# Kernel optimization log

Measured on AMD Instinct MI355X. Metric: run time of the kernel, lower is better.

## Reference

```python
import jax, jax.numpy as jnp
import numpy as np

N_HEADS = 16
EMBED_DIM = 2048
BATCH, SEQ = 2, 2048


def setup_inputs() -> dict:
    key = jax.random.key(0)
    k1, k2, k3, k4, k5 = jax.random.split(key, 5)
    s_in = 1.0 / np.sqrt(EMBED_DIM)
    return {
        "x": jax.random.normal(k1, (BATCH, SEQ, EMBED_DIM), dtype=jnp.float32),
        "w_in": jax.random.normal(k2, (3 * EMBED_DIM, EMBED_DIM), dtype=jnp.float32) * s_in,
        "b_in": jax.random.normal(k3, (3 * EMBED_DIM,), dtype=jnp.float32) * 0.02,
        "w_out": jax.random.normal(k4, (EMBED_DIM, EMBED_DIM), dtype=jnp.float32) * s_in,
        "b_out": jax.random.normal(k5, (EMBED_DIM,), dtype=jnp.float32) * 0.02,
        "causal_mask": 1,
    }


def reference(x, w_in, b_in, w_out, b_out, causal_mask):
    b, l, e = x.shape
    h, d = N_HEADS, e // N_HEADS
    qkv = x @ w_in.T + b_in                      # [b, l, 3e]
    q, k, v = jnp.split(qkv, 3, axis=-1)
    # b l (h d) -> b h l d
    q = q.reshape(b, l, h, d).transpose(0, 2, 1, 3)
    k = k.reshape(b, l, h, d).transpose(0, 2, 1, 3)
    v = v.reshape(b, l, h, d).transpose(0, 2, 1, 3)
    scores = jnp.einsum("bhqd,bhkd->bhqk", q, k) / jnp.sqrt(jnp.float32(d))
    if causal_mask:
        tri = jnp.triu(jnp.ones((l, l), dtype=bool), k=1)  # True above diagonal
        scores = jnp.where(tri, -jnp.inf, scores)
    attn = jax.nn.softmax(scores, axis=-1)
    out = jnp.einsum("bhqk,bhkd->bhqd", attn, v)  # [b, h, l, d]
    out = out.transpose(0, 2, 1, 3).reshape(b, l, e)
    return out @ w_out.T + b_out
```

## Files before the change

### kernel.cpp

```cpp
#include <hip/hip_runtime.h>
#include <hip/hip_bf16.h>
#include <math.h>

typedef __attribute__((ext_vector_type(4))) float floatx4;
typedef __attribute__((ext_vector_type(16))) float floatx16;
typedef __attribute__((ext_vector_type(8))) __bf16 bf16x8;

__device__ __forceinline__ unsigned short f2bf(float f) {
    union { float f; unsigned int u; } v; v.f = f;
    unsigned int u = v.u;
    u += 0x7FFFu + ((u >> 16) & 1u);
    return (unsigned short)(u >> 16);
}

__device__ __forceinline__ unsigned int pkbf(float a, float b) {
    return (unsigned int)f2bf(a) | ((unsigned int)f2bf(b) << 16);
}

__device__ __forceinline__ void gl_lds16(const void* g, void* l) {
    __builtin_amdgcn_global_load_lds(
        (const __attribute__((address_space(1))) void*)g,
        (__attribute__((address_space(3))) void*)l, 16, 0, 0);
}

__global__ void cast_f32_bf16(const float* __restrict__ in,
                              unsigned short* __restrict__ out, int n) {
    int i = (blockIdx.x * blockDim.x + threadIdx.x) * 4;
    if (i + 4 <= n) {
        float4 f = *(const float4*)(in + i);
        ushort4 o;
        o.x = f2bf(f.x); o.y = f2bf(f.y); o.z = f2bf(f.z); o.w = f2bf(f.w);
        *(ushort4*)(out + i) = o;
    }
}


#define VMCNT(n) asm volatile("s_waitcnt vmcnt(" #n ")" ::: "memory")
#define LGKM0()  asm volatile("s_waitcnt lgkmcnt(0)" ::: "memory")
#define BARF()   do { asm volatile("" ::: "memory"); __builtin_amdgcn_s_barrier(); \
                      asm volatile("" ::: "memory"); } while (0)

#define STAGE_A4(bsel, tt, h) do { \
    const unsigned short* _s = Ab + (size_t)((h) * 128 + rstage) * K + (tt) * 64 + scol; \
    char* _d = bufc + (bsel) * 49152 + (h) * 16384 + wid * 1024; \
    gl_lds16(_s, _d); \
    gl_lds16(_s + (size_t)64 * K, _d + 8192); \
} while (0)

#define STAGE_B4(bsel, tt, h) do { \
    const unsigned short* _s = Bb + (size_t)((h) * 64 + rstage) * K + (tt) * 64 + scol; \
    char* _d = bufc + (bsel) * 49152 + 32768 + (h) * 8192 + wid * 1024; \
    gl_lds16(_s, _d); \
} while (0)

#define STAGE_TILE(bsel, tt) do { \
    STAGE_A4(bsel, tt, 0); STAGE_A4(bsel, tt, 1); \
    STAGE_B4(bsel, tt, 0); STAGE_B4(bsel, tt, 1); \
} while (0)

#define RDA(base, ii, kse) (*(const bf16x8*)((base) + (ii) * 2048 + rdoffA + (kse)))
#define RDB(base, jj, kse) (*(const bf16x8*)((base) + (jj) * 2048 + rdoffB + (kse)))

#define MFMA_C(iofs) do { \
    __builtin_amdgcn_s_setprio(1); \
    _Pragma("unroll") \
    for (int ii = 0; ii < 4; ++ii) { \
        _Pragma("unroll") \
        for (int jj = 0; jj < 2; ++jj) { \
            acc[(iofs) + ii][jj] = __builtin_amdgcn_mfma_f32_16x16x32_bf16( \
                aF[((iofs) + ii) * 2 + 0], bL[jj * 2 + 0], acc[(iofs) + ii][jj], 0, 0, 0); \
            acc[(iofs) + ii][jj] = __builtin_amdgcn_mfma_f32_16x16x32_bf16( \
                aF[((iofs) + ii) * 2 + 1], bL[jj * 2 + 1], acc[(iofs) + ii][jj], 0, 0, 0); \
        } } \
    __builtin_amdgcn_s_setprio(0); \
} while (0)

template<int MODE>
__global__ __launch_bounds__(512, 2) void gemm4p(
    const unsigned short* __restrict__ A,
    const unsigned short* __restrict__ B,
    const float* __restrict__ bias,
    float* __restrict__ Cf,
    unsigned short* __restrict__ q_ws,
    unsigned short* __restrict__ k_ws,
    unsigned short* __restrict__ vT_ws,
    int M, int N, int K)
{
    extern __shared__ char ldsc[];
    char* const bufc = ldsc;

    const int nby = M >> 8;
    const int nwg = gridDim.x;
    const int qq = nwg >> 3;
    const int wg = (blockIdx.x & 7) * qq + (blockIdx.x >> 3);
    const int by = wg % nby, bx = wg / nby;
    const int m0 = by << 8, n0 = bx << 7;

    const int tid = threadIdx.x;
    const int lane = tid & 63, wid = tid >> 6;
    const int li = lane & 15, quad = lane >> 4;
    const int wr = wid >> 2, wc = wid & 3;

    const int rstage = tid >> 3;
    const int scol = (((tid & 7) ^ ((tid >> 3) & 7)) << 3);
    const unsigned short* Ab = A + (size_t)m0 * K;
    const unsigned short* Bb = B + (size_t)n0 * K;

    const int swz = (lane & 7) << 4;
    const int ks0 = ((quad << 4)     ) ^ swz;
    const int ks1 = ((quad << 4) + 64) ^ swz;
    const int rdoffA = li * 128;
    const int rdoffB = li * 128 + ((wc & 1) << 12);

    const char* rdA0 = bufc + wr * 16384;
    const char* rdB0 = bufc + 32768 + (wc >> 1) * 8192;
    const char* rdA1 = rdA0 + 49152;
    const char* rdB1 = rdB0 + 49152;

    floatx4 acc[8][2] = {};
    bf16x8 aF[16], bL[4];

    const int KTn = K >> 6;

    STAGE_TILE(0, 0);
    STAGE_TILE(1, 1);
    VMCNT(6);
    BARF();

    for (int t = 0; t < KTn; t += 2) {
        const bool pf = (t + 2 < KTn);

        #pragma unroll
        for (int ii = 0; ii < 8; ++ii) { aF[ii*2+0] = RDA(rdA0, ii, ks0); aF[ii*2+1] = RDA(rdA0, ii, ks1); }
        #pragma unroll
        for (int jj = 0; jj < 2; ++jj) { bL[jj*2+0] = RDB(rdB0, jj, ks0); bL[jj*2+1] = RDB(rdB0, jj, ks1); }
        BARF();
        MFMA_C(0);
        LGKM0();
        BARF();

        if (pf) STAGE_TILE(0, t + 2);
        BARF();
        MFMA_C(4);
        if (pf) { VMCNT(6); } else { VMCNT(0); }
        BARF();

        #pragma unroll
        for (int ii = 0; ii < 8; ++ii) { aF[ii*2+0] = RDA(rdA1, ii, ks0); aF[ii*2+1] = RDA(rdA1, ii, ks1); }
        #pragma unroll
        for (int jj = 0; jj < 2; ++jj) { bL[jj*2+0] = RDB(rdB1, jj, ks0); bL[jj*2+1] = RDB(rdB1, jj, ks1); }
        BARF();
        MFMA_C(0);
        LGKM0();
        BARF();

        if (pf) STAGE_TILE(1, t + 3);
        BARF();
        MFMA_C(4);
        if (pf) { VMCNT(6); } else { VMCNT(0); }
        BARF();
    }

    const int colb = wc * 32;
    const int rowb = wr * 128;
    if (MODE == 0) {
        #pragma unroll
        for (int i2 = 0; i2 < 8; ++i2)
            #pragma unroll
            for (int j2 = 0; j2 < 2; ++j2) {
                const int col = n0 + colb + j2 * 16 + li;
                const float bv = bias[col];
                #pragma unroll
                for (int r = 0; r < 4; ++r) {
                    const int row = m0 + rowb + i2 * 16 + quad * 4 + r;
                    Cf[(size_t)row * N + col] = acc[i2][j2][r] + bv;
                }
            }
    } else {
        const int which = bx >> 4;
        const int hh = bx & 15;
        const int lbase = m0 & 2047;
        const size_t bh = (size_t)((m0 >> 11) * 16 + hh);
        if (which == 2) {
            unsigned short (*Lv)[264] = (unsigned short(*)[264])ldsc;
            #pragma unroll
            for (int i2 = 0; i2 < 8; ++i2)
                #pragma unroll
                for (int j2 = 0; j2 < 2; ++j2) {
                    const int col = colb + j2 * 16 + li;
                    const float bv = bias[n0 + col];
                    #pragma unroll
                    for (int r = 0; r < 4; ++r) {
                        const int row = rowb + i2 * 16 + quad * 4 + r;
                        Lv[col][row] = f2bf(acc[i2][j2][r] + bv);
                    }
                }
            __syncthreads();
            #pragma unroll
            for (int c = 0; c < 8; ++c) {
                int chunk = c * 512 + tid;
                int d = chunk >> 5;
                int ls = (chunk & 31) * 8;
                *(uint4*)(vT_ws + (bh * 128 + d) * 2048 + lbase + ls) =
                    *(const uint4*)&Lv[d][ls];
            }
        } else {
            unsigned short (*Lq)[136] = (unsigned short(*)[136])ldsc;
            #pragma unroll
            for (int i2 = 0; i2 < 8; ++i2)
                #pragma unroll
                for (int j2 = 0; j2 < 2; ++j2) {
                    const int col = colb + j2 * 16 + li;
                    const float bv = bias[n0 + col];
                    #pragma unroll
                    for (int r = 0; r < 4; ++r) {
                        const int row = rowb + i2 * 16 + quad * 4 + r;
                        Lq[row][col] = f2bf(acc[i2][j2][r] + bv);
                    }
                }
            __syncthreads();
            unsigned short* dst = which ? k_ws : q_ws;
            #pragma unroll
            for (int c = 0; c < 8; ++c) {
                int chunk = c * 512 + tid;
                int row = chunk >> 4;
                int dc = (chunk & 15) * 8;
                *(uint4*)(dst + (bh * 2048 + lbase + row) * (size_t)128 + dc) =
                    *(const uint4*)&Lq[row][dc];
            }
        }
    }
}

#define AP 8
__global__ __launch_bounds__(256, 2) void attn_kernel(
    const unsigned short* __restrict__ q_ws,
    const unsigned short* __restrict__ k_ws,
    const unsigned short* __restrict__ vT_ws,
    unsigned short* __restrict__ aout,
    const int* __restrict__ causal_ptr)
{
    __shared__ unsigned short Ksm[128][128 + AP];
    __shared__ unsigned short Vsm[128][128 + AP];

    const int ord = blockIdx.x;
    int qt, bhid;
    if (ord < 256) { qt = ord >> 5;              bhid = ord & 31; }
    else           { qt = 15 - ((ord - 256) >> 5); bhid = ord & 31; }
    const int b = bhid >> 4, h = bhid & 15;

    const int tid = threadIdx.x;
    const int lane = tid & 63, w = tid >> 6;
    const int lq = lane & 31;
    const int half = lane >> 5;
    const size_t bh = (size_t)(b * 16 + h);
    const unsigned short* Qp = q_ws + bh * 2048 * 128;
    const unsigned short* Kp = k_ws + bh * 2048 * 128;
    const unsigned short* Vp = vT_ws + bh * 128 * 2048;
    const int causal = causal_ptr[0];
    const float scale = 0.08838834764831845f;

    const int qg = qt * 128 + w * 32 + lq;
    bf16x8 qf[8];
    #pragma unroll
    for (int s = 0; s < 8; ++s)
        qf[s] = *(const bf16x8*)(Qp + (size_t)qg * 128 + s * 16 + half * 8);

    floatx16 O[4] = {};
    float m_i = -INFINITY, l_i = 0.f;

    const int myEnd = causal ? qt : 15;
    for (int kt = 0; kt <= myEnd; ++kt) {
        #pragma unroll
        for (int c = 0; c < 8; ++c) {
            int chunk = c * 256 + tid;
            int row = chunk >> 4;
            int cc  = (chunk & 15) * 8;
            *(uint4*)(&Ksm[row][cc]) =
                *(const uint4*)(Kp + (size_t)(kt * 128 + row) * 128 + cc);
            *(uint4*)(&Vsm[row][cc]) =
                *(const uint4*)(Vp + (size_t)row * 2048 + kt * 128 + cc);
        }
        __syncthreads();

        floatx16 S[4] = {};
        #pragma unroll
        for (int ct = 0; ct < 4; ++ct)
            #pragma unroll
            for (int s = 0; s < 8; ++s) {
                bf16x8 kf = *(const bf16x8*)(&Ksm[ct * 32 + lq][s * 16 + half * 8]);
                S[ct] = __builtin_amdgcn_mfma_f32_32x32x16_bf16(kf, qf[s], S[ct], 0, 0, 0);
            }

        const bool diag = causal && (kt == qt);
        float mx = -INFINITY;
        #pragma unroll
        for (int ct = 0; ct < 4; ++ct)
            #pragma unroll
            for (int r = 0; r < 16; ++r) {
                float sv = S[ct][r] * scale;
                if (diag) {
                    int key = 32 * ct + (r & 3) + 8 * (r >> 2) + 4 * half;
                    if (kt * 128 + key > qg) sv = -INFINITY;
                }
                S[ct][r] = sv;
                mx = fmaxf(mx, sv);
            }
        mx = fmaxf(mx, __shfl_xor(mx, 32, 64));
        float m_new = fmaxf(m_i, mx);
        float m_use = (m_new == -INFINITY) ? 0.f : m_new;
        float alpha = __expf(m_i - m_use);

        float rs = 0.f;
        #pragma unroll
        for (int ct = 0; ct < 4; ++ct)
            #pragma unroll
            for (int r = 0; r < 16; ++r) {
                float p = __expf(S[ct][r] - m_use);
                S[ct][r] = p;
                rs += p;
            }
        rs += __shfl_xor(rs, 32, 64);
        l_i = l_i * alpha + rs;
        m_i = m_new;
        #pragma unroll
        for (int dt = 0; dt < 4; ++dt)
            #pragma unroll
            for (int r = 0; r < 16; ++r)
                O[dt][r] *= alpha;

        bf16x8 pfr[8];
        #pragma unroll
        for (int ct = 0; ct < 4; ++ct)
            #pragma unroll
            for (int h2 = 0; h2 < 2; ++h2) {
                int base = 8 * h2;
                unsigned int pk0 = pkbf(S[ct][base + 0], S[ct][base + 1]);
                unsigned int pk1 = pkbf(S[ct][base + 2], S[ct][base + 3]);
                unsigned int pk2 = pkbf(S[ct][base + 4], S[ct][base + 5]);
                unsigned int pk3 = pkbf(S[ct][base + 6], S[ct][base + 7]);
                unsigned int x0 = __shfl_xor((int)pk0, 32, 64);
                unsigned int x1 = __shfl_xor((int)pk1, 32, 64);
                unsigned int x2 = __shfl_xor((int)pk2, 32, 64);
                unsigned int x3 = __shfl_xor((int)pk3, 32, 64);
                union { unsigned int u[4]; bf16x8 v; } fr;
                fr.u[0] = half ? x2 : pk0;
                fr.u[1] = half ? x3 : pk1;
                fr.u[2] = half ? pk2 : x0;
                fr.u[3] = half ? pk3 : x1;
                pfr[ct * 2 + h2] = fr.v;
            }

        #pragma unroll
        for (int dt = 0; dt < 4; ++dt)
            #pragma unroll
            for (int s = 0; s < 8; ++s) {
                bf16x8 vf = *(const bf16x8*)(&Vsm[dt * 32 + lq][s * 16 + half * 8]);
                O[dt] = __builtin_amdgcn_mfma_f32_32x32x16_bf16(vf, pfr[s], O[dt], 0, 0, 0);
            }
        __syncthreads();
    }

    const float invl = 1.0f / l_i;
    #pragma unroll
    for (int dt = 0; dt < 4; ++dt)
        #pragma unroll
        for (int g = 0; g < 4; ++g) {
            int dbase = dt * 32 + g * 8 + half * 4;
            ushort4 o4;
            o4.x = f2bf(O[dt][g * 4 + 0] * invl);
            o4.y = f2bf(O[dt][g * 4 + 1] * invl);
            o4.z = f2bf(O[dt][g * 4 + 2] * invl);
            o4.w = f2bf(O[dt][g * 4 + 3] * invl);
            *(ushort4*)(&Ksm[w * 32 + lq][dbase]) = o4;
        }
    __syncthreads();
    #pragma unroll
    for (int c = 0; c < 8; ++c) {
        int chunk = c * 256 + tid;
        int row = chunk >> 4;
        int dc = (chunk & 15) * 8;
        uint4 v = *(const uint4*)(&Ksm[row][dc]);
        *(uint4*)(aout + ((size_t)b * 2048 + qt * 128 + row) * 2048 + h * 128 + dc) = v;
    }
}

extern "C" void kernel_launch(void* const* d_in, const int* in_sizes, int n_in,
                              void* d_out, int out_size, void* d_ws, size_t ws_size,
                              hipStream_t stream) {
    const float* x     = (const float*)d_in[0];
    const float* w_in  = (const float*)d_in[1];
    const float* b_in  = (const float*)d_in[2];
    const float* w_out = (const float*)d_in[3];
    const float* b_out = (const float*)d_in[4];
    const int* causal  = (const int*)d_in[5];

    char* ws = (char*)d_ws;
    unsigned short* xb    = (unsigned short*)ws; ws += (size_t)4096 * 2048 * 2;
    unsigned short* wb    = (unsigned short*)ws; ws += (size_t)6144 * 2048 * 2;
    unsigned short* wob   = (unsigned short*)ws; ws += (size_t)2048 * 2048 * 2;
    unsigned short* q_ws  = (unsigned short*)ws; ws += (size_t)32 * 2048 * 128 * 2;
    unsigned short* k_ws  = (unsigned short*)ws; ws += (size_t)32 * 2048 * 128 * 2;
    unsigned short* vT_ws = (unsigned short*)ws; ws += (size_t)32 * 2048 * 128 * 2;
    unsigned short* aout  = (unsigned short*)ws; ws += (size_t)4096 * 2048 * 2;

    static int once = []() {
        auto* f0 = gemm4p<0>;
        auto* f1 = gemm4p<1>;
        hipFuncSetAttribute((const void*)f0,
            hipFuncAttributeMaxDynamicSharedMemorySize, 98304);
        hipFuncSetAttribute((const void*)f1,
            hipFuncAttributeMaxDynamicSharedMemorySize, 98304);
        return 0;
    }();
    (void)once;

    cast_f32_bf16<<<8192, 256, 0, stream>>>(x, xb, 4096 * 2048);
    cast_f32_bf16<<<12288, 256, 0, stream>>>(w_in, wb, 6144 * 2048);
    cast_f32_bf16<<<4096, 256, 0, stream>>>(w_out, wob, 2048 * 2048);

    gemm4p<1><<<768, 512, 98304, stream>>>(
        xb, wb, b_in, nullptr, q_ws, k_ws, vT_ws, 4096, 6144, 2048);

    attn_kernel<<<512, 256, 0, stream>>>(
        q_ws, k_ws, vT_ws, aout, causal);

    gemm4p<0><<<256, 512, 98304, stream>>>(
        aout, wob, b_out, (float*)d_out, nullptr, nullptr, nullptr,
        4096, 2048, 2048);
}
```

Before: 383.4 us.

## Widen QKV GEMM tile to 256x256 and prefetch K/V tiles in attention

Adds a dedicated QKV projection kernel with 256x256 output tiles, using 128KB LDS and interleaved staging. This halves the grid to 384 workgroups and increases operand reuse per loaded tile. The attention kernel now loads the next K/V block into registers while the current block's MFMAs run, and raises wave priority around the MFMA loops. The trade-off is higher register and LDS pressure, which likely limits the QKV kernel to one workgroup per CU despite its launch bounds, plus a more complex epilogue that writes two heads per tile.

```diff
diff --git a/kernel.cpp b/kernel.cpp
--- a/kernel.cpp
+++ b/kernel.cpp
@@ -34,11 +34,223 @@
     }
 }
 
-
 #define VMCNT(n) asm volatile("s_waitcnt vmcnt(" #n ")" ::: "memory")
 #define LGKM0()  asm volatile("s_waitcnt lgkmcnt(0)" ::: "memory")
 #define BARF()   do { asm volatile("" ::: "memory"); __builtin_amdgcn_s_barrier(); \
                       asm volatile("" ::: "memory"); } while (0)
+
+#define RDA(base, ii, kse) (*(const bf16x8*)((base) + (ii) * 2048 + rdoffA + (kse)))
+#define RDB(base, jj, kse) (*(const bf16x8*)((base) + (jj) * 2048 + rdoffB + (kse)))
+
+
+#define STAGE_A8(bsel, tt, h) do { \
+    const unsigned short* _s = Ab + (size_t)((h) * 128 + rstage) * K + (tt) * 64 + scol; \
+    char* _d = bufc + (bsel) * 65536 + (h) * 16384 + wid * 1024; \
+    gl_lds16(_s, _d); \
+    gl_lds16(_s + (size_t)64 * K, _d + 8192); \
+} while (0)
+
+#define STAGE_B8(bsel, tt, h) do { \
+    const unsigned short* _s = Bb + (size_t)((h) * 128 + rstage) * K + (tt) * 64 + scol; \
+    char* _d = bufc + (bsel) * 65536 + 32768 + (h) * 16384 + wid * 1024; \
+    gl_lds16(_s, _d); \
+    gl_lds16(_s + (size_t)64 * K, _d + 8192); \
+} while (0)
+
+#define MFMA_Q(iofs, jofs, BV) do { \
+    __builtin_amdgcn_s_setprio(1); \
+    _Pragma("unroll") \
+    for (int ii = 0; ii < 4; ++ii) { \
+        _Pragma("unroll") \
+        for (int jj = 0; jj < 2; ++jj) { \
+            acc[(iofs) + ii][(jofs) + jj] = __builtin_amdgcn_mfma_f32_16x16x32_bf16( \
+                aF[ii * 2 + 0], BV[jj * 2 + 0], acc[(iofs) + ii][(jofs) + jj], 0, 0, 0); \
+            acc[(iofs) + ii][(jofs) + jj] = __builtin_amdgcn_mfma_f32_16x16x32_bf16( \
+                aF[ii * 2 + 1], BV[jj * 2 + 1], acc[(iofs) + ii][(jofs) + jj], 0, 0, 0); \
+        } } \
+    __builtin_amdgcn_s_setprio(0); \
+} while (0)
+
+__global__ __launch_bounds__(512, 2) void gemm_qkv(
+    const unsigned short* __restrict__ A,
+    const unsigned short* __restrict__ B,
+    const float* __restrict__ bias,
+    unsigned short* __restrict__ q_ws,
+    unsigned short* __restrict__ k_ws,
+    unsigned short* __restrict__ vT_ws,
+    int M, int N, int K)
+{
+    extern __shared__ char ldsc[];
+    char* const bufc = ldsc;
+
+    const int nby = M >> 8;
+    const int nwg = gridDim.x;
+    const int qq = nwg >> 3;
+    const int wg = (blockIdx.x & 7) * qq + (blockIdx.x >> 3);
+    const int by = wg % nby, bx = wg / nby;
+    const int m0 = by << 8, n0 = bx << 8;
+
+    const int tid = threadIdx.x;
+    const int lane = tid & 63, wid = tid >> 6;
+    const int li = lane & 15, quad = lane >> 4;
+    const int wr = wid >> 2, wc = wid & 3;
+
+    const int rstage = tid >> 3;
+    const int scol = (((tid & 7) ^ ((tid >> 3) & 7)) << 3);
+    const unsigned short* Ab = A + (size_t)m0 * K;
+    const unsigned short* Bb = B + (size_t)n0 * K;
+
+    const int swz = (lane & 7) << 4;
+    const int ks0 = ((quad << 4)     ) ^ swz;
+    const int ks1 = ((quad << 4) + 64) ^ swz;
+    const int rdoffA = li * 128;
+    const int rdoffB = li * 128 + ((wc & 1) << 13);
+
+    const char* rdA0 = bufc + wr * 16384;
+    const char* rdB0 = bufc + 32768 + (wc >> 1) * 16384;
+    const char* rdA1 = rdA0 + 65536;
+    const char* rdB1 = rdB0 + 65536;
+
+    floatx4 acc[8][4] = {};
+    bf16x8 aF[8], bL[4], bH[4];
+
+    const int KTn = K >> 6;
+
+    STAGE_A8(0, 0, 0); STAGE_A8(0, 0, 1); STAGE_B8(0, 0, 0); STAGE_B8(0, 0, 1);
+    STAGE_B8(1, 1, 0); STAGE_B8(1, 1, 1); STAGE_A8(1, 1, 0);
+    VMCNT(6);
+    BARF();
+
+    for (int t = 0; t < KTn; t += 2) {
+        const bool pf = (t + 2 < KTn);
+
+        #pragma unroll
+        for (int ii = 0; ii < 4; ++ii) { aF[ii*2+0] = RDA(rdA0, ii, ks0); aF[ii*2+1] = RDA(rdA0, ii, ks1); }
+        #pragma unroll
+        for (int jj = 0; jj < 2; ++jj) { bL[jj*2+0] = RDB(rdB0, jj, ks0); bL[jj*2+1] = RDB(rdB0, jj, ks1); }
+        STAGE_A8(1, t + 1, 1);
+        BARF();
+        MFMA_Q(0, 0, bL);
+        BARF();
+
+        #pragma unroll
+        for (int jj = 0; jj < 2; ++jj) { bH[jj*2+0] = RDB(rdB0, 2 + jj, ks0); bH[jj*2+1] = RDB(rdB0, 2 + jj, ks1); }
+        BARF();
+        MFMA_Q(0, 2, bH);
+        BARF();
+
+        #pragma unroll
+        for (int ii = 0; ii < 4; ++ii) { aF[ii*2+0] = RDA(rdA0, 4 + ii, ks0); aF[ii*2+1] = RDA(rdA0, 4 + ii, ks1); }
+        if (pf) STAGE_B8(0, t + 2, 0);
+        BARF();
+        MFMA_Q(4, 0, bL);
+        BARF();
+
+        if (pf) { STAGE_B8(0, t + 2, 1); STAGE_A8(0, t + 2, 0); }
+        BARF();
+        MFMA_Q(4, 2, bH);
+        if (pf) { VMCNT(6); } else { VMCNT(0); }
+        BARF();
+
+        #pragma unroll
+        for (int ii = 0; ii < 4; ++ii) { aF[ii*2+0] = RDA(rdA1, ii, ks0); aF[ii*2+1] = RDA(rdA1, ii, ks1); }
+        #pragma unroll
+        for (int jj = 0; jj < 2; ++jj) { bL[jj*2+0] = RDB(rdB1, jj, ks0); bL[jj*2+1] = RDB(rdB1, jj, ks1); }
+        if (pf) STAGE_A8(0, t + 2, 1);
+        BARF();
+        MFMA_Q(0, 0, bL);
+        BARF();
+
+        #pragma unroll
+        for (int jj = 0; jj < 2; ++jj) { bH[jj*2+0] = RDB(rdB1, 2 + jj, ks0); bH[jj*2+1] = RDB(rdB1, 2 + jj, ks1); }
+        BARF();
+        MFMA_Q(0, 2, bH);
+        BARF();
+
+        #pragma unroll
+        for (int ii = 0; ii < 4; ++ii) { aF[ii*2+0] = RDA(rdA1, 4 + ii, ks0); aF[ii*2+1] = RDA(rdA1, 4 + ii, ks1); }
+        if (pf) STAGE_B8(1, t + 3, 0);
+        BARF();
+        MFMA_Q(4, 0, bL);
+        BARF();
+
+        if (pf) { STAGE_B8(1, t + 3, 1); STAGE_A8(1, t + 3, 0); }
+        BARF();
+        MFMA_Q(4, 2, bH);
+        VMCNT(6);
+        BARF();
+    }
+
+    const int which = n0 >> 11;
+    const int h0 = (n0 & 2047) >> 7;
+    const int bb = m0 >> 11;
+    const int lbase = m0 & 2047;
+    if (which == 2) {
+        unsigned short (*Lv)[264] = (unsigned short(*)[264])ldsc;
+        #pragma unroll
+        for (int p = 0; p < 2; ++p) {
+            if ((wc >> 1) == p) {
+                #pragma unroll
+                for (int i2 = 0; i2 < 8; ++i2)
+                    #pragma unroll
+                    for (int j2 = 0; j2 < 4; ++j2) {
+                        const int col = wc * 64 + j2 * 16 + li;
+                        const float bv = bias[n0 + col];
+                        const int lc = col - p * 128;
+                        #pragma unroll
+                        for (int r = 0; r < 4; ++r) {
+                            const int row = wr * 128 + i2 * 16 + quad * 4 + r;
+                            Lv[lc][row] = f2bf(acc[i2][j2][r] + bv);
+                        }
+                    }
+            }
+            __syncthreads();
+            const size_t bh = (size_t)(bb * 16 + h0 + p);
+            #pragma unroll
+            for (int c = 0; c < 8; ++c) {
+                int chunk = c * 512 + tid;
+                int d = chunk >> 5;
+                int ls = (chunk & 31) * 8;
+                *(uint4*)(vT_ws + (bh * 128 + d) * 2048 + lbase + ls) =
+                    *(const uint4*)&Lv[d][ls];
+            }
+            if (p == 0) __syncthreads();
+        }
+    } else {
+        unsigned short* dst = which ? k_ws : q_ws;
+        unsigned short (*Lq)[136] = (unsigned short(*)[136])ldsc;
+        #pragma unroll
+        for (int p = 0; p < 2; ++p) {
+            if ((wc >> 1) == p) {
+                #pragma unroll
+                for (int i2 = 0; i2 < 8; ++i2)
+                    #pragma unroll
+                    for (int j2 = 0; j2 < 4; ++j2) {
+                        const int col = wc * 64 + j2 * 16 + li;
+                        const float bv = bias[n0 + col];
+                        const int lc = col - p * 128;
+                        #pragma unroll
+                        for (int r = 0; r < 4; ++r) {
+                            const int row = wr * 128 + i2 * 16 + quad * 4 + r;
+                            Lq[row][lc] = f2bf(acc[i2][j2][r] + bv);
+                        }
+                    }
+            }
+            __syncthreads();
+            const size_t bh = (size_t)(bb * 16 + h0 + p);
+            #pragma unroll
+            for (int c = 0; c < 8; ++c) {
+                int chunk = c * 512 + tid;
+                int row = chunk >> 4;
+                int dc = (chunk & 15) * 8;
+                *(uint4*)(dst + (bh * 2048 + (size_t)(lbase + row)) * 128 + dc) =
+                    *(const uint4*)&Lq[row][dc];
+            }
+            if (p == 0) __syncthreads();
+        }
+    }
+}
+
 
 #define STAGE_A4(bsel, tt, h) do { \
     const unsigned short* _s = Ab + (size_t)((h) * 128 + rstage) * K + (tt) * 64 + scol; \
@@ -53,13 +265,10 @@
     gl_lds16(_s, _d); \
 } while (0)
 
-#define STAGE_TILE(bsel, tt) do { \
+#define STAGE_TILE4(bsel, tt) do { \
     STAGE_A4(bsel, tt, 0); STAGE_A4(bsel, tt, 1); \
     STAGE_B4(bsel, tt, 0); STAGE_B4(bsel, tt, 1); \
 } while (0)
-
-#define RDA(base, ii, kse) (*(const bf16x8*)((base) + (ii) * 2048 + rdoffA + (kse)))
-#define RDB(base, jj, kse) (*(const bf16x8*)((base) + (jj) * 2048 + rdoffB + (kse)))
 
 #define MFMA_C(iofs) do { \
     __builtin_amdgcn_s_setprio(1); \
@@ -75,15 +284,11 @@
     __builtin_amdgcn_s_setprio(0); \
 } while (0)
 
-template<int MODE>
-__global__ __launch_bounds__(512, 2) void gemm4p(
+__global__ __launch_bounds__(512, 2) void gemm_out(
     const unsigned short* __restrict__ A,
     const unsigned short* __restrict__ B,
     const float* __restrict__ bias,
     float* __restrict__ Cf,
-    unsigned short* __restrict__ q_ws,
-    unsigned short* __restrict__ k_ws,
-    unsigned short* __restrict__ vT_ws,
     int M, int N, int K)
 {
     extern __shared__ char ldsc[];
@@ -122,8 +327,8 @@
 
     const int KTn = K >> 6;
 
-    STAGE_TILE(0, 0);
-    STAGE_TILE(1, 1);
+    STAGE_TILE4(0, 0);
+    STAGE_TILE4(1, 1);
     VMCNT(6);
     BARF();
 
@@ -139,7 +344,7 @@
         LGKM0();
         BARF();
 
-        if (pf) STAGE_TILE(0, t + 2);
+        if (pf) STAGE_TILE4(0, t + 2);
         BARF();
         MFMA_C(4);
         if (pf) { VMCNT(6); } else { VMCNT(0); }
@@ -154,7 +359,7 @@
         LGKM0();
         BARF();
 
-        if (pf) STAGE_TILE(1, t + 3);
+        if (pf) STAGE_TILE4(1, t + 3);
         BARF();
         MFMA_C(4);
         if (pf) { VMCNT(6); } else { VMCNT(0); }
@@ -163,73 +368,18 @@
 
     const int colb = wc * 32;
     const int rowb = wr * 128;
-    if (MODE == 0) {
-        #pragma unroll
-        for (int i2 = 0; i2 < 8; ++i2)
-            #pragma unroll
-            for (int j2 = 0; j2 < 2; ++j2) {
-                const int col = n0 + colb + j2 * 16 + li;
-                const float bv = bias[col];
-                #pragma unroll
-                for (int r = 0; r < 4; ++r) {
-                    const int row = m0 + rowb + i2 * 16 + quad * 4 + r;
-                    Cf[(size_t)row * N + col] = acc[i2][j2][r] + bv;
-                }
-            }
-    } else {
-        const int which = bx >> 4;
-        const int hh = bx & 15;
-        const int lbase = m0 & 2047;
-        const size_t bh = (size_t)((m0 >> 11) * 16 + hh);
-        if (which == 2) {
-            unsigned short (*Lv)[264] = (unsigned short(*)[264])ldsc;
-            #pragma unroll
-            for (int i2 = 0; i2 < 8; ++i2)
-                #pragma unroll
-                for (int j2 = 0; j2 < 2; ++j2) {
-                    const int col = colb + j2 * 16 + li;
-                    const float bv = bias[n0 + col];
-                    #pragma unroll
-                    for (int r = 0; r < 4; ++r) {
-                        const int row = rowb + i2 * 16 + quad * 4 + r;
-                        Lv[col][row] = f2bf(acc[i2][j2][r] + bv);
-                    }
-                }
-            __syncthreads();
-            #pragma unroll
-            for (int c = 0; c < 8; ++c) {
-                int chunk = c * 512 + tid;
-                int d = chunk >> 5;
-                int ls = (chunk & 31) * 8;
-                *(uint4*)(vT_ws + (bh * 128 + d) * 2048 + lbase + ls) =
-                    *(const uint4*)&Lv[d][ls];
-            }
-        } else {
-            unsigned short (*Lq)[136] = (unsigned short(*)[136])ldsc;
-            #pragma unroll
-            for (int i2 = 0; i2 < 8; ++i2)
-                #pragma unroll
-                for (int j2 = 0; j2 < 2; ++j2) {
-                    const int col = colb + j2 * 16 + li;
-                    const float bv = bias[n0 + col];
-                    #pragma unroll
-                    for (int r = 0; r < 4; ++r) {
-                        const int row = rowb + i2 * 16 + quad * 4 + r;
-                        Lq[row][col] = f2bf(acc[i2][j2][r] + bv);
-                    }
-                }
-            __syncthreads();
-            unsigned short* dst = which ? k_ws : q_ws;
-            #pragma unroll
-            for (int c = 0; c < 8; ++c) {
-                int chunk = c * 512 + tid;
-                int row = chunk >> 4;
-                int dc = (chunk & 15) * 8;
-                *(uint4*)(dst + (bh * 2048 + lbase + row) * (size_t)128 + dc) =
-                    *(const uint4*)&Lq[row][dc];
+    #pragma unroll
+    for (int i2 = 0; i2 < 8; ++i2)
+        #pragma unroll
+        for (int j2 = 0; j2 < 2; ++j2) {
+            const int col = n0 + colb + j2 * 16 + li;
+            const float bv = bias[col];
+            #pragma unroll
+            for (int r = 0; r < 4; ++r) {
+                const int row = m0 + rowb + i2 * 16 + quad * 4 + r;
+                Cf[(size_t)row * N + col] = acc[i2][j2][r] + bv;
             }
         }
-    }
 }
 
 #define AP 8
@@ -260,6 +410,9 @@
     const int causal = causal_ptr[0];
     const float scale = 0.08838834764831845f;
 
+    const int srow = tid >> 4;
+    const int scc = (tid & 15) * 8;
+
     const int qg = qt * 128 + w * 32 + lq;
     bf16x8 qf[8];
     #pragma unroll
@@ -269,21 +422,28 @@
     floatx16 O[4] = {};
     float m_i = -INFINITY, l_i = 0.f;
 
+    uint4 kr[8], vr[8];
+
+    #pragma unroll
+    for (int c = 0; c < 8; ++c) {
+        int row = c * 16 + srow;
+        kr[c] = *(const uint4*)(Kp + (size_t)row * 128 + scc);
+        vr[c] = *(const uint4*)(Vp + (size_t)row * 2048 + scc);
+    }
+    #pragma unroll
+    for (int c = 0; c < 8; ++c) {
+        int row = c * 16 + srow;
+        *(uint4*)(&Ksm[row][scc]) = kr[c];
+        *(uint4*)(&Vsm[row][scc]) = vr[c];
+    }
+    __syncthreads();
+
     const int myEnd = causal ? qt : 15;
     for (int kt = 0; kt <= myEnd; ++kt) {
-        #pragma unroll
-        for (int c = 0; c < 8; ++c) {
-            int chunk = c * 256 + tid;
-            int row = chunk >> 4;
-            int cc  = (chunk & 15) * 8;
-            *(uint4*)(&Ksm[row][cc]) =
-                *(const uint4*)(Kp + (size_t)(kt * 128 + row) * 128 + cc);
-            *(uint4*)(&Vsm[row][cc]) =
-                *(const uint4*)(Vp + (size_t)row * 2048 + kt * 128 + cc);
-        }
-        __syncthreads();
+        const bool more = (kt < myEnd);
 
         floatx16 S[4] = {};
+        __builtin_amdgcn_s_setprio(1);
         #pragma unroll
         for (int ct = 0; ct < 4; ++ct)
             #pragma unroll
@@ -291,6 +451,7 @@
                 bf16x8 kf = *(const bf16x8*)(&Ksm[ct * 32 + lq][s * 16 + half * 8]);
                 S[ct] = __builtin_amdgcn_mfma_f32_32x32x16_bf16(kf, qf[s], S[ct], 0, 0, 0);
             }
+        __builtin_amdgcn_s_setprio(0);
 
         const bool diag = causal && (kt == qt);
         float mx = -INFINITY;
@@ -351,6 +512,16 @@
                 pfr[ct * 2 + h2] = fr.v;
             }
 
+        if (more) {
+            #pragma unroll
+            for (int c = 0; c < 8; ++c) {
+                int row = c * 16 + srow;
+                kr[c] = *(const uint4*)(Kp + (size_t)((kt + 1) * 128 + row) * 128 + scc);
+                vr[c] = *(const uint4*)(Vp + (size_t)row * 2048 + (kt + 1) * 128 + scc);
+            }
+        }
+
+        __builtin_amdgcn_s_setprio(1);
         #pragma unroll
         for (int dt = 0; dt < 4; ++dt)
             #pragma unroll
@@ -358,8 +529,20 @@
                 bf16x8 vf = *(const bf16x8*)(&Vsm[dt * 32 + lq][s * 16 + half * 8]);
                 O[dt] = __builtin_amdgcn_mfma_f32_32x32x16_bf16(vf, pfr[s], O[dt], 0, 0, 0);
             }
-        __syncthreads();
-    }
+        __builtin_amdgcn_s_setprio(0);
+
+        if (more) {
+            __syncthreads();
+            #pragma unroll
+            for (int c = 0; c < 8; ++c) {
+                int row = c * 16 + srow;
+                *(uint4*)(&Ksm[row][scc]) = kr[c];
+                *(uint4*)(&Vsm[row][scc]) = vr[c];
+            }
+            __syncthreads();
+        }
+    }
+    __syncthreads();
 
     const float invl = 1.0f / l_i;
     #pragma unroll
@@ -405,11 +588,9 @@
     unsigned short* aout  = (unsigned short*)ws; ws += (size_t)4096 * 2048 * 2;
 
     static int once = []() {
-        auto* f0 = gemm4p<0>;
-        auto* f1 = gemm4p<1>;
-        hipFuncSetAttribute((const void*)f0,
-            hipFuncAttributeMaxDynamicSharedMemorySize, 98304);
-        hipFuncSetAttribute((const void*)f1,
+        hipFuncSetAttribute((const void*)gemm_qkv,
+            hipFuncAttributeMaxDynamicSharedMemorySize, 131072);
+        hipFuncSetAttribute((const void*)gemm_out,
             hipFuncAttributeMaxDynamicSharedMemorySize, 98304);
         return 0;
     }();
@@ -419,13 +600,12 @@
     cast_f32_bf16<<<12288, 256, 0, stream>>>(w_in, wb, 6144 * 2048);
     cast_f32_bf16<<<4096, 256, 0, stream>>>(w_out, wob, 2048 * 2048);
 
-    gemm4p<1><<<768, 512, 98304, stream>>>(
-        xb, wb, b_in, nullptr, q_ws, k_ws, vT_ws, 4096, 6144, 2048);
+    gemm_qkv<<<384, 512, 131072, stream>>>(
+        xb, wb, b_in, q_ws, k_ws, vT_ws, 4096, 6144, 2048);
 
     attn_kernel<<<512, 256, 0, stream>>>(
         q_ws, k_ws, vT_ws, aout, causal);
 
-    gemm4p<0><<<256, 512, 98304, stream>>>(
-        aout, wob, b_out, (float*)d_out, nullptr, nullptr, nullptr,
-        4096, 2048, 2048);
-}
+    gemm_out<<<256, 512, 98304, stream>>>(
+        aout, wob, b_out, (float*)d_out, 4096, 2048, 2048);
+}
```

Result: slower. 479.9 us (+25.2%).

## Double-buffer K/V tiles in attention kernel via register prefetch

Applied to the files above, without the earlier changes.

The attention kernel now keeps two K/V tile buffers in dynamic shared memory and prefetches the next tile into registers while the current tile's MFMAs run, then writes it to the alternate buffer. This removes one barrier per iteration and hides global-load latency behind compute. The cost is 136 KB of LDS per block and launch bounds dropped to one block per CU, so occupancy halves. It also adds 64 extra VGPRs of staging registers.

```diff
diff --git a/kernel.cpp b/kernel.cpp
--- a/kernel.cpp
+++ b/kernel.cpp
@@ -232,16 +232,15 @@
     }
 }
 
-#define AP 8
-__global__ __launch_bounds__(256, 2) void attn_kernel(
+__global__ __launch_bounds__(256, 1) void attn_kernel(
     const unsigned short* __restrict__ q_ws,
     const unsigned short* __restrict__ k_ws,
     const unsigned short* __restrict__ vT_ws,
     unsigned short* __restrict__ aout,
     const int* __restrict__ causal_ptr)
 {
-    __shared__ unsigned short Ksm[128][128 + AP];
-    __shared__ unsigned short Vsm[128][128 + AP];
+    extern __shared__ char asmem[];
+    unsigned short* const S0 = (unsigned short*)asmem;
 
     const int ord = blockIdx.x;
     int qt, bhid;
@@ -260,6 +259,9 @@
     const int causal = causal_ptr[0];
     const float scale = 0.08838834764831845f;
 
+    const int srow = tid >> 4;
+    const int scc  = (tid & 15) * 8;
+
     const int qg = qt * 128 + w * 32 + lq;
     bf16x8 qf[8];
     #pragma unroll
@@ -269,26 +271,43 @@
     floatx16 O[4] = {};
     float m_i = -INFINITY, l_i = 0.f;
 
+    uint4 kr[8], vr[8];
+
+    #pragma unroll
+    for (int c = 0; c < 8; ++c) {
+        int row = c * 16 + srow;
+        kr[c] = *(const uint4*)(Kp + (size_t)row * 128 + scc);
+        vr[c] = *(const uint4*)(Vp + (size_t)row * 2048 + scc);
+    }
+    #pragma unroll
+    for (int c = 0; c < 8; ++c) {
+        int row = c * 16 + srow;
+        *(uint4*)(S0 + row * 136 + scc) = kr[c];
+        *(uint4*)(S0 + 17408 + row * 136 + scc) = vr[c];
+    }
+    __syncthreads();
+
     const int myEnd = causal ? qt : 15;
     for (int kt = 0; kt <= myEnd; ++kt) {
-        #pragma unroll
-        for (int c = 0; c < 8; ++c) {
-            int chunk = c * 256 + tid;
-            int row = chunk >> 4;
-            int cc  = (chunk & 15) * 8;
-            *(uint4*)(&Ksm[row][cc]) =
-                *(const uint4*)(Kp + (size_t)(kt * 128 + row) * 128 + cc);
-            *(uint4*)(&Vsm[row][cc]) =
-                *(const uint4*)(Vp + (size_t)row * 2048 + kt * 128 + cc);
+        unsigned short* const Ksc = S0 + (kt & 1) * 34816;
+        unsigned short* const Vsc = Ksc + 17408;
+        const bool more = (kt < myEnd);
+
+        if (more) {
+            #pragma unroll
+            for (int c = 0; c < 8; ++c) {
+                int row = c * 16 + srow;
+                kr[c] = *(const uint4*)(Kp + (size_t)((kt + 1) * 128 + row) * 128 + scc);
+                vr[c] = *(const uint4*)(Vp + (size_t)row * 2048 + (kt + 1) * 128 + scc);
+            }
         }
-        __syncthreads();
 
         floatx16 S[4] = {};
         #pragma unroll
         for (int ct = 0; ct < 4; ++ct)
             #pragma unroll
             for (int s = 0; s < 8; ++s) {
-                bf16x8 kf = *(const bf16x8*)(&Ksm[ct * 32 + lq][s * 16 + half * 8]);
+                bf16x8 kf = *(const bf16x8*)(Ksc + (ct * 32 + lq) * 136 + s * 16 + half * 8);
                 S[ct] = __builtin_amdgcn_mfma_f32_32x32x16_bf16(kf, qf[s], S[ct], 0, 0, 0);
             }
 
@@ -355,12 +374,23 @@
         for (int dt = 0; dt < 4; ++dt)
             #pragma unroll
             for (int s = 0; s < 8; ++s) {
-                bf16x8 vf = *(const bf16x8*)(&Vsm[dt * 32 + lq][s * 16 + half * 8]);
+                bf16x8 vf = *(const bf16x8*)(Vsc + (dt * 32 + lq) * 136 + s * 16 + half * 8);
                 O[dt] = __builtin_amdgcn_mfma_f32_32x32x16_bf16(vf, pfr[s], O[dt], 0, 0, 0);
             }
+
+        if (more) {
+            unsigned short* const Kn = S0 + ((kt + 1) & 1) * 34816;
+            #pragma unroll
+            for (int c = 0; c < 8; ++c) {
+                int row = c * 16 + srow;
+                *(uint4*)(Kn + row * 136 + scc) = kr[c];
+                *(uint4*)(Kn + 17408 + row * 136 + scc) = vr[c];
+            }
+        }
         __syncthreads();
     }
 
+    unsigned short* const Ep = S0;
     const float invl = 1.0f / l_i;
     #pragma unroll
     for (int dt = 0; dt < 4; ++dt)
@@ -372,7 +402,7 @@
             o4.y = f2bf(O[dt][g * 4 + 1] * invl);
             o4.z = f2bf(O[dt][g * 4 + 2] * invl);
             o4.w = f2bf(O[dt][g * 4 + 3] * invl);
-            *(ushort4*)(&Ksm[w * 32 + lq][dbase]) = o4;
+            *(ushort4*)(Ep + (w * 32 + lq) * 136 + dbase) = o4;
         }
     __syncthreads();
     #pragma unroll
@@ -380,7 +410,7 @@
         int chunk = c * 256 + tid;
         int row = chunk >> 4;
         int dc = (chunk & 15) * 8;
-        uint4 v = *(const uint4*)(&Ksm[row][dc]);
+        uint4 v = *(const uint4*)(Ep + row * 136 + dc);
         *(uint4*)(aout + ((size_t)b * 2048 + qt * 128 + row) * 2048 + h * 128 + dc) = v;
     }
 }
@@ -411,6 +441,8 @@
             hipFuncAttributeMaxDynamicSharedMemorySize, 98304);
         hipFuncSetAttribute((const void*)f1,
             hipFuncAttributeMaxDynamicSharedMemorySize, 98304);
+        hipFuncSetAttribute((const void*)attn_kernel,
+            hipFuncAttributeMaxDynamicSharedMemorySize, 139264);
         return 0;
     }();
     (void)once;
@@ -422,7 +454,7 @@
     gemm4p<1><<<768, 512, 98304, stream>>>(
         xb, wb, b_in, nullptr, q_ws, k_ws, vT_ws, 4096, 6144, 2048);
 
-    attn_kernel<<<512, 256, 0, stream>>>(
+    attn_kernel<<<512, 256, 139264, stream>>>(
         q_ws, k_ws, vT_ws, aout, causal);
 
     gemm4p<0><<<256, 512, 98304, stream>>>(
```

After: 452.1 us. +17.9%, slower.

## Double-buffer attention K/V tiles with async global-to-LDS loads and XOR swizzle

Applied to the files above, without the earlier changes.

The attention kernel now loads K and V tiles straight into LDS with global_load_lds into two 64KB buffers. The next tile is prefetched while the current one is computed, using vmcnt waits and barriers. The LDS layout drops row padding and uses an XOR swizzle to avoid bank conflicts. The cost is 128KB of dynamic LDS per block, which cuts occupancy from two blocks per CU to one.

```diff
diff --git a/kernel.cpp b/kernel.cpp
--- a/kernel.cpp
+++ b/kernel.cpp
@@ -232,16 +232,14 @@
     }
 }
 
-#define AP 8
-__global__ __launch_bounds__(256, 2) void attn_kernel(
+__global__ __launch_bounds__(256, 1) void attn_kernel(
     const unsigned short* __restrict__ q_ws,
     const unsigned short* __restrict__ k_ws,
     const unsigned short* __restrict__ vT_ws,
     unsigned short* __restrict__ aout,
     const int* __restrict__ causal_ptr)
 {
-    __shared__ unsigned short Ksm[128][128 + AP];
-    __shared__ unsigned short Vsm[128][128 + AP];
+    extern __shared__ char asmem[];
 
     const int ord = blockIdx.x;
     int qt, bhid;
@@ -260,6 +258,23 @@
     const int causal = causal_ptr[0];
     const float scale = 0.08838834764831845f;
 
+    const int trow = tid >> 4;
+    const int sco  = (((tid & 15) ^ (tid >> 4)) << 3);
+    const int widB = (tid >> 6) * 1024;
+    const int rsw = (lq & 15) << 3;
+
+#define ATTN_STAGE(bsel, ktile) do { \
+    char* _kd = asmem + (bsel) * 65536 + widB; \
+    char* _vd = _kd + 32768; \
+    const unsigned short* _ks = Kp + (size_t)((ktile) * 128 + trow) * 128 + sco; \
+    const unsigned short* _vs = Vp + (size_t)trow * 2048 + (ktile) * 128 + sco; \
+    _Pragma("unroll") \
+    for (int _c = 0; _c < 8; ++_c) { \
+        gl_lds16(_ks + (size_t)_c * 2048,  _kd + _c * 4096); \
+        gl_lds16(_vs + (size_t)_c * 32768, _vd + _c * 4096); \
+    } \
+} while (0)
+
     const int qg = qt * 128 + w * 32 + lq;
     bf16x8 qf[8];
     #pragma unroll
@@ -270,25 +285,22 @@
     float m_i = -INFINITY, l_i = 0.f;
 
     const int myEnd = causal ? qt : 15;
+
+    ATTN_STAGE(0, 0);
+    if (myEnd >= 1) { ATTN_STAGE(1, 1); VMCNT(16); }
+    else            { VMCNT(0); }
+    BARF();
+
     for (int kt = 0; kt <= myEnd; ++kt) {
-        #pragma unroll
-        for (int c = 0; c < 8; ++c) {
-            int chunk = c * 256 + tid;
-            int row = chunk >> 4;
-            int cc  = (chunk & 15) * 8;
-            *(uint4*)(&Ksm[row][cc]) =
-                *(const uint4*)(Kp + (size_t)(kt * 128 + row) * 128 + cc);
-            *(uint4*)(&Vsm[row][cc]) =
-                *(const uint4*)(Vp + (size_t)row * 2048 + kt * 128 + cc);
-        }
-        __syncthreads();
+        const unsigned short* Ksc = (const unsigned short*)(asmem + (kt & 1) * 65536);
+        const unsigned short* Vsc = Ksc + 16384;
 
         floatx16 S[4] = {};
         #pragma unroll
         for (int ct = 0; ct < 4; ++ct)
             #pragma unroll
             for (int s = 0; s < 8; ++s) {
-                bf16x8 kf = *(const bf16x8*)(&Ksm[ct * 32 + lq][s * 16 + half * 8]);
+                bf16x8 kf = *(const bf16x8*)(Ksc + (ct * 32 + lq) * 128 + ((s * 16 + half * 8) ^ rsw));
                 S[ct] = __builtin_amdgcn_mfma_f32_32x32x16_bf16(kf, qf[s], S[ct], 0, 0, 0);
             }
 
@@ -355,12 +367,21 @@
         for (int dt = 0; dt < 4; ++dt)
             #pragma unroll
             for (int s = 0; s < 8; ++s) {
-                bf16x8 vf = *(const bf16x8*)(&Vsm[dt * 32 + lq][s * 16 + half * 8]);
+                bf16x8 vf = *(const bf16x8*)(Vsc + (dt * 32 + lq) * 128 + ((s * 16 + half * 8) ^ rsw));
                 O[dt] = __builtin_amdgcn_mfma_f32_32x32x16_bf16(vf, pfr[s], O[dt], 0, 0, 0);
             }
-        __syncthreads();
+
+        BARF();
+        if (kt + 2 <= myEnd) {
+            ATTN_STAGE(kt & 1, kt + 2);
+            VMCNT(16);
+        } else {
+            VMCNT(0);
+        }
+        BARF();
     }
 
+    unsigned short* const Ep = (unsigned short*)asmem;
     const float invl = 1.0f / l_i;
     #pragma unroll
     for (int dt = 0; dt < 4; ++dt)
@@ -372,7 +393,7 @@
             o4.y = f2bf(O[dt][g * 4 + 1] * invl);
             o4.z = f2bf(O[dt][g * 4 + 2] * invl);
             o4.w = f2bf(O[dt][g * 4 + 3] * invl);
-            *(ushort4*)(&Ksm[w * 32 + lq][dbase]) = o4;
+            *(ushort4*)(Ep + (w * 32 + lq) * 136 + dbase) = o4;
         }
     __syncthreads();
     #pragma unroll
@@ -380,9 +401,10 @@
         int chunk = c * 256 + tid;
         int row = chunk >> 4;
         int dc = (chunk & 15) * 8;
-        uint4 v = *(const uint4*)(&Ksm[row][dc]);
+        uint4 v = *(const uint4*)(Ep + row * 136 + dc);
         *(uint4*)(aout + ((size_t)b * 2048 + qt * 128 + row) * 2048 + h * 128 + dc) = v;
     }
+#undef ATTN_STAGE
 }
 
 extern "C" void kernel_launch(void* const* d_in, const int* in_sizes, int n_in,
@@ -411,6 +433,8 @@
             hipFuncAttributeMaxDynamicSharedMemorySize, 98304);
         hipFuncSetAttribute((const void*)f1,
             hipFuncAttributeMaxDynamicSharedMemorySize, 98304);
+        hipFuncSetAttribute((const void*)attn_kernel,
+            hipFuncAttributeMaxDynamicSharedMemorySize, 131072);
         return 0;
     }();
     (void)once;
@@ -422,7 +446,7 @@
     gemm4p<1><<<768, 512, 98304, stream>>>(
         xb, wb, b_in, nullptr, q_ws, k_ws, vT_ws, 4096, 6144, 2048);
 
-    attn_kernel<<<512, 256, 0, stream>>>(
+    attn_kernel<<<512, 256, 131072, stream>>>(
         q_ws, k_ws, vT_ws, aout, causal);
 
     gemm4p<0><<<256, 512, 98304, stream>>>(
```

New measurement: 390.4 us. Within noise of the previous version (+1.8%).
